# Kernel tuning notes

Hardware: AMD Instinct MI355X
Metric: run time of the kernel (lower is better)

Reference implementation:

```python
import jax, jax.numpy as jnp
import numpy as np

N, L, V, D, E, A, HOP, NL = 256, 128, 50000, 300, 512, 256, 4, 7


def _lstm(x, Wih, Whh, bih, bhh):
    # x: [B, T, Din]; torch gate order i, f, g, o. Returns [B, T, H].
    B = x.shape[0]
    H = Whh.shape[1]
    xg = jnp.einsum('btd,gd->btg', x, Wih) + bih + bhh  # precompute input projections
    h0 = jnp.zeros((B, H), x.dtype)
    c0 = jnp.zeros((B, H), x.dtype)

    def step(carry, xt):
        h, c = carry
        g = xt + h @ Whh.T
        i, f, gg, o = jnp.split(g, 4, axis=-1)
        c = jax.nn.sigmoid(f) * c + jax.nn.sigmoid(i) * jnp.tanh(gg)
        h = jax.nn.sigmoid(o) * jnp.tanh(c)
        return (h, c), h

    _, hs = jax.lax.scan(step, (h0, c0), jnp.swapaxes(xg, 0, 1))
    return jnp.swapaxes(hs, 0, 1)


def _bilstm(x, fwd, bwd):
    hf = _lstm(x, *fwd)
    hb = jnp.flip(_lstm(jnp.flip(x, 1), *bwd), 1)
    return jnp.concatenate([hf, hb], axis=-1)


def setup_inputs() -> dict:
    key = jax.random.key(0)
    ks = jax.random.split(key, 20)
    r = lambda k, shape, fan: jax.random.normal(k, shape, jnp.float32) / np.float32(np.sqrt(fan))
    F = 2 * E * HOP  # sentence feature after hop-attention flatten
    z = lambda n: jnp.zeros((n,), jnp.float32)
    inp = {
        'tokens': jax.random.randint(ks[0], (N, L), 0, V),
        'lengths': jax.random.randint(ks[1], (N,), 1, L + 1).astype(jnp.int32),
        'embedding': r(ks[2], (V, D), D),
        'tok_Wih_f': r(ks[3], (4 * E, D), D), 'tok_Whh_f': r(ks[4], (4 * E, E), E),
        'tok_bih_f': z(4 * E), 'tok_bhh_f': z(4 * E),
        'tok_Wih_b': r(ks[5], (4 * E, D), D), 'tok_Whh_b': r(ks[6], (4 * E, E), E),
        'tok_bih_b': z(4 * E), 'tok_bhh_b': z(4 * E),
        'attn_W': r(ks[7], (A, 2 * E), 2 * E), 'attn_b': z(A),
        'attn_ctx': r(ks[8], (HOP, A), A),
        'sent_Wih_f': r(ks[9], (4 * E, F), F), 'sent_Whh_f': r(ks[10], (4 * E, E), E),
        'sent_bih_f': z(4 * E), 'sent_bhh_f': z(4 * E),
        'sent_Wih_b': r(ks[11], (4 * E, F), F), 'sent_Whh_b': r(ks[12], (4 * E, E), E),
        'sent_bih_b': z(4 * E), 'sent_bhh_b': z(4 * E),
        'lin_W': r(ks[13], (NL, 2 * E), 2 * E), 'lin_b': z(NL),
    }
    return inp


def reference(tokens, lengths, embedding, tok_Wih_f, tok_Whh_f, tok_bih_f, tok_bhh_f,
              tok_Wih_b, tok_Whh_b, tok_bih_b, tok_bhh_b,
              attn_W, attn_b, attn_ctx,
              sent_Wih_f, sent_Whh_f, sent_bih_f, sent_bhh_f,
              sent_Wih_b, sent_Whh_b, sent_bih_b, sent_bhh_b,
              lin_W, lin_b):
    n, l = tokens.shape
    emb = embedding[tokens]  # [N, L, D] (pad token id 0 embedded, as in original pad_sequence)
    enc = _bilstm(emb, (tok_Wih_f, tok_Whh_f, tok_bih_f, tok_bhh_f),
                  (tok_Wih_b, tok_Whh_b, tok_bih_b, tok_bhh_b))  # [N, L, 2E]
    hidden = jnp.einsum('nle,ae->nla', enc, attn_W) + attn_b      # [N, L, A]
    scores = jnp.einsum('nla,ha->nlh', hidden, attn_ctx)          # [N, L, HOP]
    attn = jax.nn.softmax(scores, axis=-1)  # softmax over hops (torch dim=1 on [L,hop])
    mask = (jnp.arange(l)[None, :] < lengths[:, None]).astype(enc.dtype)[:, :, None]
    sent = jnp.einsum('nle,nlh->neh', enc, attn * mask)           # [N, 2E, HOP]
    sent = sent.reshape(1, n, -1)                                 # [1, N, 2E*HOP]
    out = _bilstm(sent, (sent_Wih_f, sent_Whh_f, sent_bih_f, sent_bhh_f),
                  (sent_Wih_b, sent_Whh_b, sent_bih_b, sent_bhh_b))[0]  # [N, 2E]
    return out @ lin_W.T + lin_b  # [N, n_labels]
```

## Files before the change

### kernel.cpp

```cpp
#include <hip/hip_runtime.h>


typedef _Float16 f16;
typedef _Float16 f16x8 __attribute__((ext_vector_type(8)));
typedef float f32x4 __attribute__((ext_vector_type(4)));

#define DI __device__ __forceinline__

DI float sigm(float x) { return 1.f / (1.f + __expf(-x)); }
DI float tanh_(float x) { return 2.f / (1.f + __expf(-2.f * x)) - 1.f; }

#define GLDS16(g, l)                                                        \
  __builtin_amdgcn_global_load_lds(                                         \
      (const __attribute__((address_space(1))) void*)(const void*)(g),      \
      (__attribute__((address_space(3))) void*)(l), 16, 0, 0)

constexpr size_t O_EMBH  = 0;
constexpr size_t O_ENC   = O_EMBH  + 20971520;
constexpr size_t O_HBUF  = O_ENC   + 67108864;
constexpr size_t O_AW    = O_HBUF  + 1048576;
constexpr size_t O_CTXW  = O_AW    + 524288;
constexpr size_t O_SENTH = O_CTXW  + 16640;
constexpr size_t O_XGS   = O_SENTH + 2097152;
constexpr size_t O_HSBUF = O_XGS   + 4194304;
constexpr size_t O_OUTS  = O_HSBUF + 8192;
constexpr size_t O_FLAGS = O_OUTS  + 1048576;
constexpr size_t TOTAL_WS = O_FLAGS + 2048;

__global__ __launch_bounds__(256) void sentinel_kernel(float* out, int n) {
  for (int i = threadIdx.x; i < n; i += 256) out[i] = 1.0e4f;
}

__global__ __launch_bounds__(256) void embed_kernel(
    const int* __restrict__ tokens, const float* __restrict__ emb,
    f16* __restrict__ out) {
  const int row = blockIdx.x * 4 + (threadIdx.x >> 6);
  const int lane = threadIdx.x & 63;
  const long tok = tokens[row];
  const float* src = emb + tok * 300;
  f16* dst = out + (long)row * 320;
  for (int c = lane; c < 320; c += 64)
    dst[c] = (c < 300) ? (f16)src[c] : (f16)0.f;
}

__global__ __launch_bounds__(256) void ctxw_kernel(
    const float* __restrict__ W, const float* __restrict__ b,
    const float* __restrict__ ctx, float* __restrict__ ctxW,
    float* __restrict__ cb) {
  const int h = blockIdx.x, tid = threadIdx.x;
  f32x4 acc = {0.f, 0.f, 0.f, 0.f};
  for (int a = 0; a < 256; ++a) {
    const float c = ctx[h * 256 + a];
    const f32x4 w4 = *(const f32x4*)&W[(long)a * 1024 + tid * 4];
    acc[0] += c * w4[0]; acc[1] += c * w4[1];
    acc[2] += c * w4[2]; acc[3] += c * w4[3];
  }
  *(f32x4*)&ctxW[h * 1024 + tid * 4] = acc;
  if (tid == 0) {
    float s = 0.f;
    for (int a = 0; a < 256; ++a) s += ctx[h * 256 + a] * b[a];
    cb[h] = s;
  }
}

DI void wg_barrier(int* fl, int slot, int poll_idx, int target, int tid,
                   int wave) {
  __syncthreads();
  if (tid == 0)
    __hip_atomic_store(&fl[slot], target, __ATOMIC_RELEASE,
                       __HIP_MEMORY_SCOPE_AGENT);
  if (wave == 0) {
    while (__hip_atomic_load(&fl[poll_idx], __ATOMIC_RELAXED,
                             __HIP_MEMORY_SCOPE_AGENT) < target) {}
    __builtin_amdgcn_fence(__ATOMIC_ACQUIRE, "agent");
  }
  __syncthreads();
}

constexpr int WIH_OFF = 65536;
constexpr int GBUF_OFF = 106496;
constexpr int BIAS_OFF = 122880;
constexpr int TOK_LDS = 123136;

__global__ __launch_bounds__(512) void tok_lstm(
    const f16* __restrict__ emb, const float* __restrict__ Whh_f,
    const float* __restrict__ Whh_b, const float* __restrict__ Wih_f,
    const float* __restrict__ Wih_b, const float* __restrict__ bih_f,
    const float* __restrict__ bhh_f, const float* __restrict__ bih_b,
    const float* __restrict__ bhh_b, f16* __restrict__ h_buf,
    f16* __restrict__ enc, int* __restrict__ flags) {
  extern __shared__ char smem[];
  float* gbuf = (float*)(smem + GBUF_OFF);
  float* bias_s = (float*)(smem + BIAS_OFF);
  const int wg = blockIdx.x;
  const int dir = wg >> 7, rest = wg & 127;
  const int mt = rest >> 5, js = rest & 31;
  const int tid = threadIdx.x, lane = tid & 63, wave = tid >> 6;
  const float* Whh = dir ? Whh_b : Whh_f;
  const float* Wih = dir ? Wih_b : Wih_f;
  const float* bih = dir ? bih_b : bih_f;
  const float* bhh = dir ? bhh_b : bhh_f;

  for (int idx = tid; idx < 64 * 64; idx += 512) {
    const int r = idx >> 6, c8 = idx & 63;
    const int grow = (r >> 4) * 512 + js * 16 + (r & 15);
    const float* src = Whh + (long)grow * 512 + c8 * 8;
    f16x8 v;
#pragma unroll
    for (int i = 0; i < 8; ++i) v[i] = (f16)src[i];
    *(f16x8*)(smem + ((r * 1024 + c8 * 16) ^ ((r & 7) << 4))) = v;
  }
  for (int idx = tid; idx < 64 * 40; idx += 512) {
    const int r = idx / 40, c8 = idx % 40;
    const int grow = (r >> 4) * 512 + js * 16 + (r & 15);
    const int k0 = c8 * 8;
    f16x8 v;
#pragma unroll
    for (int i = 0; i < 8; ++i)
      v[i] = (k0 + i < 300) ? (f16)Wih[(long)grow * 300 + k0 + i] : (f16)0.f;
    *(f16x8*)(smem + WIH_OFF + ((r * 640 + c8 * 16) ^ ((r & 7) << 4))) = v;
  }
  if (tid < 64) {
    const int grow = (tid >> 4) * 512 + js * 16 + (tid & 15);
    bias_s[tid] = bih[grow] + bhh[grow];
  }
  __syncthreads();

  const int wm = wave & 1;
  const int wn = wave >> 1;
  const int al = lane & 15, koff = (lane >> 4) * 8;
  const int arow_base = mt * 64 + wm * 32;
  const int brow = wn * 16 + al;
  const int bswz = (brow & 7) << 4;
  const int uj = tid & 15, sg = tid >> 4;
  float c_reg[2] = {0.f, 0.f};
  int* fl = flags + dir * 128 + mt * 32;
  const int poll_idx = lane & 31;

  for (int s = 0; s < 128; ++s) {
    const int t = dir ? (127 - s) : s;
    f32x4 acc0 = {0.f, 0.f, 0.f, 0.f}, acc1 = {0.f, 0.f, 0.f, 0.f};
    {
      const long e0 = ((long)(arow_base + al) * 128 + t) * 320;
      const long e1 = e0 + 16L * 128 * 320;
#pragma unroll
      for (int kt = 0; kt < 10; ++kt) {
        const f16x8 a0 = *(const f16x8*)&emb[e0 + kt * 32 + koff];
        const f16x8 a1 = *(const f16x8*)&emb[e1 + kt * 32 + koff];
        const f16x8 bf = *(const f16x8*)(
            smem + WIH_OFF + ((brow * 640 + kt * 64 + koff * 2) ^ bswz));
        acc0 = __builtin_amdgcn_mfma_f32_16x16x32_f16(a0, bf, acc0, 0, 0, 0);
        acc1 = __builtin_amdgcn_mfma_f32_16x16x32_f16(a1, bf, acc1, 0, 0, 0);
      }
    }
    if (s > 0) {
      const f16* hb =
          h_buf + ((long)(dir * 2 + ((s - 1) & 1)) * 256 + arow_base) * 512;
#pragma unroll
      for (int kt = 0; kt < 16; ++kt) {
        const f16x8 a0 = *(const f16x8*)&hb[al * 512 + kt * 32 + koff];
        const f16x8 a1 = *(const f16x8*)&hb[(al + 16) * 512 + kt * 32 + koff];
        const f16x8 bf = *(const f16x8*)(
            smem + ((brow * 1024 + kt * 64 + koff * 2) ^ bswz));
        acc0 = __builtin_amdgcn_mfma_f32_16x16x32_f16(a0, bf, acc0, 0, 0, 0);
        acc1 = __builtin_amdgcn_mfma_f32_16x16x32_f16(a1, bf, acc1, 0, 0, 0);
      }
    }
#pragma unroll
    for (int r = 0; r < 4; ++r) {
      gbuf[(wm * 32 + (lane >> 4) * 4 + r) * 64 + wn * 16 + al] = acc0[r];
      gbuf[(wm * 32 + 16 + (lane >> 4) * 4 + r) * 64 + wn * 16 + al] = acc1[r];
    }
    __syncthreads();
#pragma unroll
    for (int e = 0; e < 2; ++e) {
      const int lr = sg * 2 + e;
      const float gi = gbuf[lr * 64 + uj] + bias_s[uj];
      const float gf = gbuf[lr * 64 + 16 + uj] + bias_s[16 + uj];
      const float gg = gbuf[lr * 64 + 32 + uj] + bias_s[32 + uj];
      const float go = gbuf[lr * 64 + 48 + uj] + bias_s[48 + uj];
      const float c = sigm(gf) * c_reg[e] + sigm(gi) * tanh_(gg);
      c_reg[e] = c;
      const float h = sigm(go) * tanh_(c);
      const int sent = mt * 64 + lr;
      h_buf[((long)(dir * 2 + (s & 1)) * 256 + sent) * 512 + js * 16 + uj] =
          (f16)h;
      enc[((long)sent * 128 + t) * 1024 + dir * 512 + js * 16 + uj] = (f16)h;
    }
    wg_barrier(fl, js, poll_idx, s + 1, tid, wave);
  }
}

__global__ __launch_bounds__(256) void attn_scores(
    const f16* __restrict__ enc, const float* __restrict__ ctxW,
    const float* __restrict__ cb, const int* __restrict__ lengths,
    float* __restrict__ aw) {
  const int row = blockIdx.x * 4 + (threadIdx.x >> 6);
  const int lane = threadIdx.x & 63;
  const f16* ep = enc + (long)row * 1024 + lane * 16;
  const f16x8 ev0 = *(const f16x8*)ep;
  const f16x8 ev1 = *(const f16x8*)(ep + 8);
  float ef[16];
#pragma unroll
  for (int i = 0; i < 8; ++i) { ef[i] = (float)ev0[i]; ef[8 + i] = (float)ev1[i]; }
  float p[4];
#pragma unroll
  for (int h = 0; h < 4; ++h) {
    const float* cw = ctxW + h * 1024 + lane * 16;
    float s = 0.f;
#pragma unroll
    for (int q = 0; q < 4; ++q) {
      const f32x4 c4 = *(const f32x4*)(cw + q * 4);
      s += ef[q * 4] * c4[0] + ef[q * 4 + 1] * c4[1] + ef[q * 4 + 2] * c4[2] +
           ef[q * 4 + 3] * c4[3];
    }
    p[h] = s;
  }
#pragma unroll
  for (int h = 0; h < 4; ++h)
#pragma unroll
    for (int off = 32; off; off >>= 1) p[h] += __shfl_xor(p[h], off);
  if (lane == 0) {
#pragma unroll
    for (int h = 0; h < 4; ++h) p[h] += cb[h];
    const float m = fmaxf(fmaxf(p[0], p[1]), fmaxf(p[2], p[3]));
    const float e0 = __expf(p[0] - m), e1 = __expf(p[1] - m),
                e2 = __expf(p[2] - m), e3 = __expf(p[3] - m);
    const int n = row >> 7, l = row & 127;
    const float keep = (l < lengths[n]) ? 1.f / (e0 + e1 + e2 + e3) : 0.f;
    ((f32x4*)aw)[row] = (f32x4){e0 * keep, e1 * keep, e2 * keep, e3 * keep};
  }
}

__global__ __launch_bounds__(256) void attn_pool(const f16* __restrict__ enc,
                                                 const float* __restrict__ aw,
                                                 f16* __restrict__ sent) {
  const int n = blockIdx.x;
  __shared__ float aw_s[512];
  for (int i = threadIdx.x; i < 512; i += 256) aw_s[i] = aw[n * 512 + i];
  __syncthreads();
  const int e0 = threadIdx.x;
  float acc[4][4] = {};
  const f16* ep = enc + (long)n * 128 * 1024;
  for (int l = 0; l < 128; ++l) {
    const float a0 = aw_s[l * 4], a1 = aw_s[l * 4 + 1], a2 = aw_s[l * 4 + 2],
                a3 = aw_s[l * 4 + 3];
#pragma unroll
    for (int q = 0; q < 4; ++q) {
      const float evx = (float)ep[l * 1024 + e0 + q * 256];
      acc[q][0] += evx * a0;
      acc[q][1] += evx * a1;
      acc[q][2] += evx * a2;
      acc[q][3] += evx * a3;
    }
  }
#pragma unroll
  for (int q = 0; q < 4; ++q) {
    const int e = e0 + q * 256;
#pragma unroll
    for (int h = 0; h < 4; ++h) sent[(long)n * 4096 + e * 4 + h] = (f16)acc[q][h];
  }
}

__global__ __launch_bounds__(256) void gemm_a16_b32(
    const f16* __restrict__ A, const float* __restrict__ B,
    float* __restrict__ C, int M, int N, int K, int lda, int ldb, int ldc) {
  __shared__ f16 As[128 * 32];
  __shared__ f16 Bs[128 * 32];
  const int tid = threadIdx.x;
  const int lane = tid & 63, wave = tid >> 6;
  const int bm = blockIdx.x, bn = blockIdx.y;
  const int wm = (wave >> 1) * 64, wn = (wave & 1) * 64;
  f32x4 acc[4][4] = {};
  const long arow0 = (long)bm * 128;
  const long brow0 = (long)bn * 128;
  const int r_half = tid >> 2;
  const int c_half = (tid & 3) * 8;
  const int brow_s = tid >> 1, bcol_s = (tid & 1) * 16;
  const int KT = K >> 5;
  for (int kt = 0; kt < KT; ++kt) {
    const int k0 = kt << 5;
#pragma unroll
    for (int i = 0; i < 2; ++i)
      GLDS16(A + (arow0 + i * 64 + r_half) * lda + k0 + c_half,
             (char*)As + i * 4096 + tid * 16);
    {
      const float* bp = B + (brow0 + brow_s) * (long)ldb + k0 + bcol_s;
      f16x8 lo, hi;
#pragma unroll
      for (int i = 0; i < 8; ++i) { lo[i] = (f16)bp[i]; hi[i] = (f16)bp[8 + i]; }
      *(f16x8*)&Bs[brow_s * 32 + bcol_s] = lo;
      *(f16x8*)&Bs[brow_s * 32 + bcol_s + 8] = hi;
    }
    __syncthreads();
    f16x8 af[4], bf[4];
    const int kr = (lane >> 4) * 8;
#pragma unroll
    for (int f = 0; f < 4; ++f) {
      af[f] = *(const f16x8*)&As[(wm + f * 16 + (lane & 15)) * 32 + kr];
      bf[f] = *(const f16x8*)&Bs[(wn + f * 16 + (lane & 15)) * 32 + kr];
    }
#pragma unroll
    for (int a = 0; a < 4; ++a)
#pragma unroll
      for (int b = 0; b < 4; ++b)
        acc[a][b] =
            __builtin_amdgcn_mfma_f32_16x16x32_f16(af[a], bf[b], acc[a][b], 0, 0, 0);
    __syncthreads();
  }
#pragma unroll
  for (int a = 0; a < 4; ++a)
#pragma unroll
    for (int r = 0; r < 4; ++r) {
      const long row = arow0 + wm + a * 16 + (lane >> 4) * 4 + r;
#pragma unroll
      for (int b = 0; b < 4; ++b) {
        const int col = bn * 128 + wn + b * 16 + (lane & 15);
        C[row * (long)ldc + col] = acc[a][b][r];
      }
    }
}

__global__ __launch_bounds__(256) void sent_lstm(
    const float* __restrict__ xgs, const float* __restrict__ Whh_f,
    const float* __restrict__ Whh_b, const float* __restrict__ bih_f,
    const float* __restrict__ bhh_f, const float* __restrict__ bih_b,
    const float* __restrict__ bhh_b, float* __restrict__ h_buf,
    float* __restrict__ outp, int* __restrict__ flags) {
  __shared__ f16 Ws[512 * 33];
  __shared__ float h_s[512];
  __shared__ float partials[256];
  __shared__ float gates_s[32];
  __shared__ float bias_s[32];
  const int wg = blockIdx.x;
  const int dir = wg >> 6, w = wg & 63;
  const int tid = threadIdx.x, lane = tid & 63, wave = tid >> 6;
  const float* Whh = dir ? Whh_b : Whh_f;
  const float* bih = dir ? bih_b : bih_f;
  const float* bhh = dir ? bhh_b : bhh_f;
  const float* xg = xgs + (long)dir * 256 * 2048;

  for (int r = 0; r < 32; ++r) {
    const int grow = (r >> 3) * 512 + w * 8 + (r & 7);
    for (int k = tid; k < 512; k += 256)
      Ws[k * 33 + r] = (f16)Whh[(long)grow * 512 + k];
  }
  if (tid < 32) {
    const int grow = (tid >> 3) * 512 + w * 8 + (tid & 7);
    bias_s[tid] = bih[grow] + bhh[grow];
  }
  __syncthreads();

  const int o = tid & 31, kq = tid >> 5;
  float c_reg = 0.f;
  int* fl = flags + 256 + dir * 64;
  const int poll_idx = lane & 63;

  for (int s = 0; s < 256; ++s) {
    const int seq = dir ? (255 - s) : s;
    if (s > 0) {
      const float* hsrc = h_buf + (dir * 2 + ((s - 1) & 1)) * 512;
      if (tid < 128) ((f32x4*)h_s)[tid] = ((const f32x4*)hsrc)[tid];
      __syncthreads();
      float acc = 0.f;
#pragma unroll 8
      for (int i = 0; i < 64; ++i) {
        const int kc = kq * 64 + i;
        acc += (float)Ws[kc * 33 + o] * h_s[kc];
      }
      partials[tid] = acc;
      __syncthreads();
      if (tid < 32) {
        float g = 0.f;
#pragma unroll
        for (int q = 0; q < 8; ++q) g += partials[q * 32 + tid];
        gates_s[tid] = g;
      }
    } else {
      if (tid < 32) gates_s[tid] = 0.f;
    }
    __syncthreads();
    if (tid < 8) {
      const int j = tid;
      const long xb = (long)seq * 2048 + w * 8 + j;
      const float gi = gates_s[j] + bias_s[j] + xg[xb];
      const float gf = gates_s[8 + j] + bias_s[8 + j] + xg[xb + 512];
      const float gg = gates_s[16 + j] + bias_s[16 + j] + xg[xb + 1024];
      const float go = gates_s[24 + j] + bias_s[24 + j] + xg[xb + 1536];
      const float c = sigm(gf) * c_reg + sigm(gi) * tanh_(gg);
      c_reg = c;
      const float h = sigm(go) * tanh_(c);
      h_buf[(dir * 2 + (s & 1)) * 512 + w * 8 + j] = h;
      outp[(long)seq * 1024 + dir * 512 + w * 8 + j] = h;
    }
    wg_barrier(fl, w, poll_idx, s + 1, tid, wave);
  }
}

__global__ __launch_bounds__(64) void final_linear(const float* __restrict__ hin,
                                                   const float* __restrict__ W,
                                                   const float* __restrict__ b,
                                                   float* __restrict__ out) {
  const int row = blockIdx.x, lane = threadIdx.x;
  float p[7] = {};
  for (int k = lane; k < 1024; k += 64) {
    const float hv = hin[row * 1024 + k];
#pragma unroll
    for (int oo = 0; oo < 7; ++oo) p[oo] += hv * W[oo * 1024 + k];
  }
#pragma unroll
  for (int oo = 0; oo < 7; ++oo)
#pragma unroll
    for (int off = 32; off; off >>= 1) p[oo] += __shfl_xor(p[oo], off);
  if (lane == 0)
#pragma unroll
    for (int oo = 0; oo < 7; ++oo) out[row * 7 + oo] = p[oo] + b[oo];
}

extern "C" void kernel_launch(void* const* d_in, const int* in_sizes, int n_in,
                              void* d_out, int out_size, void* d_ws,
                              size_t ws_size, hipStream_t stream) {
  const int* tokens = (const int*)d_in[0];
  const int* lengths = (const int*)d_in[1];
  const float* embed = (const float*)d_in[2];
  const float* tWih_f = (const float*)d_in[3];
  const float* tWhh_f = (const float*)d_in[4];
  const float* tbih_f = (const float*)d_in[5];
  const float* tbhh_f = (const float*)d_in[6];
  const float* tWih_b = (const float*)d_in[7];
  const float* tWhh_b = (const float*)d_in[8];
  const float* tbih_b = (const float*)d_in[9];
  const float* tbhh_b = (const float*)d_in[10];
  const float* attnW = (const float*)d_in[11];
  const float* attnB = (const float*)d_in[12];
  const float* attnCtx = (const float*)d_in[13];
  const float* sWih_f = (const float*)d_in[14];
  const float* sWhh_f = (const float*)d_in[15];
  const float* sbih_f = (const float*)d_in[16];
  const float* sbhh_f = (const float*)d_in[17];
  const float* sWih_b = (const float*)d_in[18];
  const float* sWhh_b = (const float*)d_in[19];
  const float* sbih_b = (const float*)d_in[20];
  const float* sbhh_b = (const float*)d_in[21];
  const float* linW = (const float*)d_in[22];
  const float* linB = (const float*)d_in[23];
  float* out = (float*)d_out;
  char* ws = (char*)d_ws;
  if (ws_size < TOTAL_WS) {
    sentinel_kernel<<<1, 256, 0, stream>>>(out, out_size);
    return;
  }

  f16* emb_h = (f16*)(ws + O_EMBH);
  f16* enc = (f16*)(ws + O_ENC);
  f16* h_buf = (f16*)(ws + O_HBUF);
  float* aw = (float*)(ws + O_AW);
  float* ctxW = (float*)(ws + O_CTXW);
  float* cb = ctxW + 4096;
  f16* sent_h = (f16*)(ws + O_SENTH);
  float* xgs = (float*)(ws + O_XGS);
  float* hs_buf = (float*)(ws + O_HSBUF);
  float* out_sent = (float*)(ws + O_OUTS);
  int* flags = (int*)(ws + O_FLAGS);

  hipFuncSetAttribute((const void*)tok_lstm,
                      hipFuncAttributeMaxDynamicSharedMemorySize, TOK_LDS);

  hipMemsetAsync(ws + O_FLAGS, 0, 2048, stream);

  embed_kernel<<<8192, 256, 0, stream>>>(tokens, embed, emb_h);
  ctxw_kernel<<<4, 256, 0, stream>>>(attnW, attnB, attnCtx, ctxW, cb);

  tok_lstm<<<256, 512, TOK_LDS, stream>>>(
      emb_h, tWhh_f, tWhh_b, tWih_f, tWih_b, tbih_f, tbhh_f, tbih_b, tbhh_b,
      h_buf, enc, flags);

  attn_scores<<<8192, 256, 0, stream>>>(enc, ctxW, cb, lengths, aw);
  attn_pool<<<256, 256, 0, stream>>>(enc, aw, sent_h);

  gemm_a16_b32<<<dim3(2, 16), 256, 0, stream>>>(
      sent_h, sWih_f, xgs, 256, 2048, 4096, 4096, 4096, 2048);
  gemm_a16_b32<<<dim3(2, 16), 256, 0, stream>>>(
      sent_h, sWih_b, xgs + 256 * 2048, 256, 2048, 4096, 4096, 4096, 2048);

  sent_lstm<<<128, 256, 0, stream>>>(xgs, sWhh_f, sWhh_b, sbih_f, sbhh_f,
                                     sbih_b, sbhh_b, hs_buf, out_sent, flags);

  final_linear<<<256, 64, 0, stream>>>(out_sent, linW, linB, out);
}
```

Before: 5.074 ms.

## Replace release/acquire barrier fences with device-scope atomic h exchange in LSTMs

The grid barrier drops its release store and acquire fence and uses relaxed flag operations instead. Visibility of the hidden state is handled by writing and reading the recurrent h buffers through relaxed agent-scope atomic loads and stores on packed 32-bit words. Separately, the token LSTM's MFMA tiling changes so each wave handles 16 rows by 32 gate columns, and each thread now computes two adjacent hidden units and stores them packed. The intent is to avoid the cost of full cache fences at every timestep. The risk is relying on relaxed ordering, which is not formally guaranteed to make the h writes visible before the flag update.

```diff
diff --git a/kernel.cpp b/kernel.cpp
--- a/kernel.cpp
+++ b/kernel.cpp
@@ -4,16 +4,21 @@
 typedef _Float16 f16;
 typedef _Float16 f16x8 __attribute__((ext_vector_type(8)));
 typedef float f32x4 __attribute__((ext_vector_type(4)));
+typedef unsigned int u32x4 __attribute__((ext_vector_type(4)));
 
 #define DI __device__ __forceinline__
 
 DI float sigm(float x) { return 1.f / (1.f + __expf(-x)); }
 DI float tanh_(float x) { return 2.f / (1.f + __expf(-2.f * x)) - 1.f; }
 
-#define GLDS16(g, l)                                                        \
-  __builtin_amdgcn_global_load_lds(                                         \
-      (const __attribute__((address_space(1))) void*)(const void*)(g),      \
-      (__attribute__((address_space(3))) void*)(l), 16, 0, 0)
+DI void st_dev(unsigned int* p, unsigned int v) {
+  __hip_atomic_store(p, v, __ATOMIC_RELAXED, __HIP_MEMORY_SCOPE_AGENT);
+}
+DI unsigned int ld_dev(const unsigned int* p) {
+  return __hip_atomic_load(p, __ATOMIC_RELAXED, __HIP_MEMORY_SCOPE_AGENT);
+}
+
+#define MFMA16(a, b, c) __builtin_amdgcn_mfma_f32_16x16x32_f16(a, b, c, 0, 0, 0)
 
 constexpr size_t O_EMBH  = 0;
 constexpr size_t O_ENC   = O_EMBH  + 20971520;
@@ -67,12 +72,11 @@
                    int wave) {
   __syncthreads();
   if (tid == 0)
-    __hip_atomic_store(&fl[slot], target, __ATOMIC_RELEASE,
+    __hip_atomic_store(&fl[slot], target, __ATOMIC_RELAXED,
                        __HIP_MEMORY_SCOPE_AGENT);
   if (wave == 0) {
     while (__hip_atomic_load(&fl[poll_idx], __ATOMIC_RELAXED,
                              __HIP_MEMORY_SCOPE_AGENT) < target) {}
-    __builtin_amdgcn_fence(__ATOMIC_ACQUIRE, "agent");
   }
   __syncthreads();
 }
@@ -87,7 +91,7 @@
     const float* __restrict__ Whh_b, const float* __restrict__ Wih_f,
     const float* __restrict__ Wih_b, const float* __restrict__ bih_f,
     const float* __restrict__ bhh_f, const float* __restrict__ bih_b,
-    const float* __restrict__ bhh_b, f16* __restrict__ h_buf,
+    const float* __restrict__ bhh_b, unsigned int* __restrict__ hbw,
     f16* __restrict__ enc, int* __restrict__ flags) {
   extern __shared__ char smem[];
   float* gbuf = (float*)(smem + GBUF_OFF);
@@ -126,66 +130,85 @@
   }
   __syncthreads();
 
-  const int wm = wave & 1;
-  const int wn = wave >> 1;
-  const int al = lane & 15, koff = (lane >> 4) * 8;
-  const int arow_base = mt * 64 + wm * 32;
-  const int brow = wn * 16 + al;
-  const int bswz = (brow & 7) << 4;
-  const int uj = tid & 15, sg = tid >> 4;
-  float c_reg[2] = {0.f, 0.f};
+  const int wm = wave >> 1;
+  const int wn = wave & 1;
+  const int al = lane & 15, kq = lane >> 4;
+  const int arow = mt * 64 + wm * 16 + al;
+  const int lr = tid >> 3, jp = tid & 7;
+  float c0 = 0.f, c1 = 0.f;
   int* fl = flags + dir * 128 + mt * 32;
   const int poll_idx = lane & 31;
 
   for (int s = 0; s < 128; ++s) {
-    const int t = dir ? (127 - s) : s;
-    f32x4 acc0 = {0.f, 0.f, 0.f, 0.f}, acc1 = {0.f, 0.f, 0.f, 0.f};
+    const int t = dir ? 127 - s : s;
+    unsigned int aw[64];
+    if (s > 0) {
+      const int base =
+          ((dir * 2 + ((s - 1) & 1)) * 256 + arow) * 256 + kq * 4;
+#pragma unroll
+      for (int kt = 0; kt < 16; ++kt)
+#pragma unroll
+        for (int w2 = 0; w2 < 4; ++w2)
+          aw[kt * 4 + w2] = ld_dev(&hbw[base + kt * 16 + w2]);
+    }
+    f32x4 acc[2] = {{0.f, 0.f, 0.f, 0.f}, {0.f, 0.f, 0.f, 0.f}};
     {
-      const long e0 = ((long)(arow_base + al) * 128 + t) * 320;
-      const long e1 = e0 + 16L * 128 * 320;
+      const long e0 = ((long)arow * 128 + t) * 320 + kq * 8;
 #pragma unroll
       for (int kt = 0; kt < 10; ++kt) {
-        const f16x8 a0 = *(const f16x8*)&emb[e0 + kt * 32 + koff];
-        const f16x8 a1 = *(const f16x8*)&emb[e1 + kt * 32 + koff];
-        const f16x8 bf = *(const f16x8*)(
-            smem + WIH_OFF + ((brow * 640 + kt * 64 + koff * 2) ^ bswz));
-        acc0 = __builtin_amdgcn_mfma_f32_16x16x32_f16(a0, bf, acc0, 0, 0, 0);
-        acc1 = __builtin_amdgcn_mfma_f32_16x16x32_f16(a1, bf, acc1, 0, 0, 0);
+        const f16x8 a = *(const f16x8*)&emb[e0 + kt * 32];
+#pragma unroll
+        for (int fb = 0; fb < 2; ++fb) {
+          const int brow = wn * 32 + fb * 16 + al;
+          const f16x8 bf = *(const f16x8*)(
+              smem + WIH_OFF +
+              ((brow * 640 + kt * 64 + kq * 16) ^ ((brow & 7) << 4)));
+          acc[fb] = MFMA16(a, bf, acc[fb]);
+        }
       }
     }
     if (s > 0) {
-      const f16* hb =
-          h_buf + ((long)(dir * 2 + ((s - 1) & 1)) * 256 + arow_base) * 512;
 #pragma unroll
       for (int kt = 0; kt < 16; ++kt) {
-        const f16x8 a0 = *(const f16x8*)&hb[al * 512 + kt * 32 + koff];
-        const f16x8 a1 = *(const f16x8*)&hb[(al + 16) * 512 + kt * 32 + koff];
-        const f16x8 bf = *(const f16x8*)(
-            smem + ((brow * 1024 + kt * 64 + koff * 2) ^ bswz));
-        acc0 = __builtin_amdgcn_mfma_f32_16x16x32_f16(a0, bf, acc0, 0, 0, 0);
-        acc1 = __builtin_amdgcn_mfma_f32_16x16x32_f16(a1, bf, acc1, 0, 0, 0);
+        u32x4 wv = {aw[kt * 4], aw[kt * 4 + 1], aw[kt * 4 + 2], aw[kt * 4 + 3]};
+        const f16x8 a = __builtin_bit_cast(f16x8, wv);
+#pragma unroll
+        for (int fb = 0; fb < 2; ++fb) {
+          const int brow = wn * 32 + fb * 16 + al;
+          const f16x8 bf = *(const f16x8*)(
+              smem + ((brow * 1024 + kt * 64 + kq * 16) ^ ((brow & 7) << 4)));
+          acc[fb] = MFMA16(a, bf, acc[fb]);
+        }
       }
     }
 #pragma unroll
-    for (int r = 0; r < 4; ++r) {
-      gbuf[(wm * 32 + (lane >> 4) * 4 + r) * 64 + wn * 16 + al] = acc0[r];
-      gbuf[(wm * 32 + 16 + (lane >> 4) * 4 + r) * 64 + wn * 16 + al] = acc1[r];
-    }
+    for (int fb = 0; fb < 2; ++fb)
+#pragma unroll
+      for (int r = 0; r < 4; ++r)
+        gbuf[(wm * 16 + kq * 4 + r) * 64 + wn * 32 + fb * 16 + al] =
+            acc[fb][r];
     __syncthreads();
-#pragma unroll
-    for (int e = 0; e < 2; ++e) {
-      const int lr = sg * 2 + e;
-      const float gi = gbuf[lr * 64 + uj] + bias_s[uj];
-      const float gf = gbuf[lr * 64 + 16 + uj] + bias_s[16 + uj];
-      const float gg = gbuf[lr * 64 + 32 + uj] + bias_s[32 + uj];
-      const float go = gbuf[lr * 64 + 48 + uj] + bias_s[48 + uj];
-      const float c = sigm(gf) * c_reg[e] + sigm(gi) * tanh_(gg);
-      c_reg[e] = c;
-      const float h = sigm(go) * tanh_(c);
+    {
+      const int j0 = jp * 2;
+      const float i0 = gbuf[lr * 64 + j0] + bias_s[j0];
+      const float i1 = gbuf[lr * 64 + j0 + 1] + bias_s[j0 + 1];
+      const float f0 = gbuf[lr * 64 + 16 + j0] + bias_s[16 + j0];
+      const float f1 = gbuf[lr * 64 + 16 + j0 + 1] + bias_s[16 + j0 + 1];
+      const float g0 = gbuf[lr * 64 + 32 + j0] + bias_s[32 + j0];
+      const float g1 = gbuf[lr * 64 + 32 + j0 + 1] + bias_s[32 + j0 + 1];
+      const float o0 = gbuf[lr * 64 + 48 + j0] + bias_s[48 + j0];
+      const float o1 = gbuf[lr * 64 + 48 + j0 + 1] + bias_s[48 + j0 + 1];
+      c0 = sigm(f0) * c0 + sigm(i0) * tanh_(g0);
+      c1 = sigm(f1) * c1 + sigm(i1) * tanh_(g1);
+      const float h0 = sigm(o0) * tanh_(c0);
+      const float h1 = sigm(o1) * tanh_(c1);
+      union { f16 h2[2]; unsigned int u; } pk;
+      pk.h2[0] = (f16)h0; pk.h2[1] = (f16)h1;
       const int sent = mt * 64 + lr;
-      h_buf[((long)(dir * 2 + (s & 1)) * 256 + sent) * 512 + js * 16 + uj] =
-          (f16)h;
-      enc[((long)sent * 128 + t) * 1024 + dir * 512 + js * 16 + uj] = (f16)h;
+      st_dev(&hbw[((dir * 2 + (s & 1)) * 256 + sent) * 256 + js * 8 + jp],
+             pk.u);
+      ((unsigned int*)enc)[((long)sent * 128 + t) * 512 + dir * 256 + js * 8 +
+                           jp] = pk.u;
     }
     wg_barrier(fl, js, poll_idx, s + 1, tid, wave);
   }
@@ -261,6 +284,11 @@
     for (int h = 0; h < 4; ++h) sent[(long)n * 4096 + e * 4 + h] = (f16)acc[q][h];
   }
 }
+
+#define GLDS16(g, l)                                                        \
+  __builtin_amdgcn_global_load_lds(                                         \
+      (const __attribute__((address_space(1))) void*)(const void*)(g),      \
+      (__attribute__((address_space(3))) void*)(l), 16, 0, 0)
 
 __global__ __launch_bounds__(256) void gemm_a16_b32(
     const f16* __restrict__ A, const float* __restrict__ B,
@@ -304,8 +332,7 @@
     for (int a = 0; a < 4; ++a)
 #pragma unroll
       for (int b = 0; b < 4; ++b)
-        acc[a][b] =
-            __builtin_amdgcn_mfma_f32_16x16x32_f16(af[a], bf[b], acc[a][b], 0, 0, 0);
+        acc[a][b] = MFMA16(af[a], bf[b], acc[a][b]);
     __syncthreads();
   }
 #pragma unroll
@@ -325,7 +352,7 @@
     const float* __restrict__ xgs, const float* __restrict__ Whh_f,
     const float* __restrict__ Whh_b, const float* __restrict__ bih_f,
     const float* __restrict__ bhh_f, const float* __restrict__ bih_b,
-    const float* __restrict__ bhh_b, float* __restrict__ h_buf,
+    const float* __restrict__ bhh_b, unsigned int* __restrict__ hsw,
     float* __restrict__ outp, int* __restrict__ flags) {
   __shared__ f16 Ws[512 * 33];
   __shared__ float h_s[512];
@@ -359,8 +386,11 @@
   for (int s = 0; s < 256; ++s) {
     const int seq = dir ? (255 - s) : s;
     if (s > 0) {
-      const float* hsrc = h_buf + (dir * 2 + ((s - 1) & 1)) * 512;
-      if (tid < 128) ((f32x4*)h_s)[tid] = ((const f32x4*)hsrc)[tid];
+      const int hb = (dir * 2 + ((s - 1) & 1)) * 512;
+      for (int q = tid; q < 512; q += 256) {
+        const unsigned int u = ld_dev(&hsw[hb + q]);
+        h_s[q] = __builtin_bit_cast(float, u);
+      }
       __syncthreads();
       float acc = 0.f;
 #pragma unroll 8
@@ -390,7 +420,8 @@
       const float c = sigm(gf) * c_reg + sigm(gi) * tanh_(gg);
       c_reg = c;
       const float h = sigm(go) * tanh_(c);
-      h_buf[(dir * 2 + (s & 1)) * 512 + w * 8 + j] = h;
+      st_dev(&hsw[(dir * 2 + (s & 1)) * 512 + w * 8 + j],
+             __builtin_bit_cast(unsigned int, h));
       outp[(long)seq * 1024 + dir * 512 + w * 8 + j] = h;
     }
     wg_barrier(fl, w, poll_idx, s + 1, tid, wave);
@@ -453,13 +484,13 @@
 
   f16* emb_h = (f16*)(ws + O_EMBH);
   f16* enc = (f16*)(ws + O_ENC);
-  f16* h_buf = (f16*)(ws + O_HBUF);
+  unsigned int* hbw = (unsigned int*)(ws + O_HBUF);
   float* aw = (float*)(ws + O_AW);
   float* ctxW = (float*)(ws + O_CTXW);
   float* cb = ctxW + 4096;
   f16* sent_h = (f16*)(ws + O_SENTH);
   float* xgs = (float*)(ws + O_XGS);
-  float* hs_buf = (float*)(ws + O_HSBUF);
+  unsigned int* hsw = (unsigned int*)(ws + O_HSBUF);
   float* out_sent = (float*)(ws + O_OUTS);
   int* flags = (int*)(ws + O_FLAGS);
 
@@ -473,7 +504,7 @@
 
   tok_lstm<<<256, 512, TOK_LDS, stream>>>(
       emb_h, tWhh_f, tWhh_b, tWih_f, tWih_b, tbih_f, tbhh_f, tbih_b, tbhh_b,
-      h_buf, enc, flags);
+      hbw, enc, flags);
 
   attn_scores<<<8192, 256, 0, stream>>>(enc, ctxW, cb, lengths, aw);
   attn_pool<<<256, 256, 0, stream>>>(enc, aw, sent_h);
@@ -484,7 +515,7 @@
       sent_h, sWih_b, xgs + 256 * 2048, 256, 2048, 4096, 4096, 4096, 2048);
 
   sent_lstm<<<128, 256, 0, stream>>>(xgs, sWhh_f, sWhh_b, sbih_f, sbhh_f,
-                                     sbih_b, sbhh_b, hs_buf, out_sent, flags);
+                                     sbih_b, sbhh_b, hsw, out_sent, flags);
 
   final_linear<<<256, 64, 0, stream>>>(out_sent, linW, linB, out);
 }
```

Result: faster. 4.212 ms (-17.0%).
